# Optimization experiments

Measured on AMD Instinct MI355X. Metric: run time of the kernel, lower is better.

The kernel has to match this reference:

```python
import jax, jax.numpy as jnp
import numpy as np

V, E, H, C, L, S, NL = 50257, 512, 1024, 1024, 1024, 2048, 2


def setup_inputs() -> dict:
    key = jax.random.key(0)
    ks = jax.random.split(key, 28)
    w = 0.02  # weight init scale
    def n(k, shape, s=1.0):
        return jax.random.normal(k, shape, dtype=jnp.float32) * s
    return {
        'input_ids': jax.random.randint(ks[0], (1,), 0, V, dtype=jnp.int32),
        'h0': n(ks[1], (NL, 1, H)),
        'c0': n(ks[2], (NL, 1, H)),
        'left_context': n(ks[3], (S, C)),
        'right_context': n(ks[4], (S, C)),
        'lemma_outputs': n(ks[5], (S, L)),
        # parameters
        'embedding': n(ks[6], (V, E), w),
        'W_ih0': n(ks[7], (4 * H, E), w), 'W_hh0': n(ks[8], (4 * H, H), w),
        'b_ih0': n(ks[9], (4 * H,), w), 'b_hh0': n(ks[10], (4 * H,), w),
        'W_ih1': n(ks[11], (4 * H, H), w), 'W_hh1': n(ks[12], (4 * H, H), w),
        'b_ih1': n(ks[13], (4 * H,), w), 'b_hh1': n(ks[14], (4 * H,), w),
        'W_left': n(ks[15], (H, C), w), 'b_left': n(ks[16], (H,), w),
        'W_right': n(ks[17], (H, C), w), 'b_right': n(ks[18], (H,), w),
        'W_lemma': n(ks[19], (H, L), w), 'b_lemma': n(ks[20], (H,), w),
        'W_concat': n(ks[21], (H, H + 2 * C + L), w), 'b_concat': n(ks[22], (H,), w),
        'W_out': n(ks[23], (V, H), w), 'b_out': n(ks[24], (V,), w),
    }


def _lstm_step(x, h, c, W_ih, W_hh, b_ih, b_hh):
    # torch LSTM gate order: i, f, g, o
    g = x @ W_ih.T + b_ih + h @ W_hh.T + b_hh  # [1, 4H]
    i, f, gg, o = jnp.split(g, 4, axis=-1)
    i = jax.nn.sigmoid(i); f = jax.nn.sigmoid(f)
    gg = jnp.tanh(gg); o = jax.nn.sigmoid(o)
    c_new = f * c + i * gg
    h_new = o * jnp.tanh(c_new)
    return h_new, c_new


def _attend(ctx, W, b, q):
    # ctx: [S, C], q: [1, H] -> Luong-style attention
    e = (ctx @ W.T + b) @ q.T          # [S, 1]
    a = jax.nn.softmax(e[:, 0])        # [S]
    return (a @ ctx)[None, :]          # [1, C]


def reference(input_ids, h0, c0, left_context, right_context, lemma_outputs,
              embedding, W_ih0, W_hh0, b_ih0, b_hh0, W_ih1, W_hh1, b_ih1, b_hh1,
              W_left, b_left, W_right, b_right, W_lemma, b_lemma,
              W_concat, b_concat, W_out, b_out):
    x = embedding[input_ids]  # [1, E]  (dropout p=0 -> identity)
    h_0, c_0 = _lstm_step(x, h0[0], c0[0], W_ih0, W_hh0, b_ih0, b_hh0)
    h_1, c_1 = _lstm_step(h_0, h0[1], c0[1], W_ih1, W_hh1, b_ih1, b_hh1)
    rnn_output = h_1  # [1, H]
    lcontext = _attend(left_context, W_left, b_left, rnn_output)
    rcontext = _attend(right_context, W_right, b_right, rnn_output)
    lemma_ctx = _attend(lemma_outputs, W_lemma, b_lemma, rnn_output)
    concat_in = jnp.concatenate([rnn_output, lcontext, rcontext, lemma_ctx], axis=-1)
    concat_out = jnp.tanh(concat_in @ W_concat.T + b_concat)  # [1, H]
    output = concat_out @ W_out.T + b_out                      # [1, V]
    h_new = jnp.stack([h_0, h_1], axis=0)  # [NL, 1, H]
    c_new = jnp.stack([c_0, c_1], axis=0)
    return output, h_new, c_new
```

## Files before the change

### kernel.cpp

```cpp
#include <hip/hip_runtime.h>
#include <hip/hip_bf16.h>
#include <math.h>


#define WS_H0        0
#define WS_CONCAT_IN 1024
#define WS_CTXOUT    2048
#define WS_V         5120
#define WS_E         8192
#define WS_COUT      20480
#define OUT_V        50257

__device__ __forceinline__ float wave_sum(float v) {
#pragma unroll
    for (int o = 32; o > 0; o >>= 1) v += __shfl_down(v, o, 64);
    return v;
}

__device__ __forceinline__ float dot4(float4 a, float4 b) {
    return a.x * b.x + a.y * b.y + a.z * b.z + a.w * b.w;
}

__device__ __forceinline__ float sigmoidf_(float x) {
    return 1.0f / (1.0f + expf(-x));
}

template <int N4E>
__global__ __launch_bounds__(256) void lstm_kernel(
    const float* __restrict__ x_base, const int* __restrict__ ids,
    const float* __restrict__ W_ih, const float* __restrict__ W_hh,
    const float* __restrict__ b_ih, const float* __restrict__ b_hh,
    const float* __restrict__ hprev, const float* __restrict__ cprev,
    float* __restrict__ h_ws, float* __restrict__ h_out, float* __restrict__ c_out,
    float* __restrict__ zero_base, int zero_count)
{
    if (zero_base != nullptr) {
        int idx = blockIdx.x * 256 + threadIdx.x;
        if (idx < zero_count) zero_base[idx] = 0.0f;
    }

    const float* x = (ids != nullptr) ? (x_base + (size_t)(4 * N4E) * (size_t)ids[0]) : x_base;

    const int k = blockIdx.x;
    const int w = threadIdx.x >> 6;
    const int lane = threadIdx.x & 63;
    const int row = w * 1024 + k;

    float acc = 0.0f;
    {
        const float4* r4 = (const float4*)(W_ih + (size_t)row * (4 * N4E));
        const float4* x4 = (const float4*)x;
#pragma unroll
        for (int j = 0; j < N4E / 64; ++j)
            acc += dot4(r4[lane + 64 * j], x4[lane + 64 * j]);
    }
    {
        const float4* r4 = (const float4*)(W_hh + (size_t)row * 1024);
        const float4* h4 = (const float4*)hprev;
#pragma unroll
        for (int j = 0; j < 4; ++j)
            acc += dot4(r4[lane + 64 * j], h4[lane + 64 * j]);
    }
    acc = wave_sum(acc);

    __shared__ float g[4];
    if (lane == 0) g[w] = acc + b_ih[row] + b_hh[row];
    __syncthreads();
    if (threadIdx.x == 0) {
        float i_ = sigmoidf_(g[0]);
        float f_ = sigmoidf_(g[1]);
        float g_ = tanhf(g[2]);
        float o_ = sigmoidf_(g[3]);
        float c_new = f_ * cprev[k] + i_ * g_;
        float h_new = o_ * tanhf(c_new);
        h_ws[k] = h_new;
        h_out[k] = h_new;
        c_out[k] = c_new;
    }
}

__global__ __launch_bounds__(256) void attn_v_kernel(
    const float* __restrict__ W0, const float* __restrict__ W1,
    const float* __restrict__ W2, const float* __restrict__ q,
    float* __restrict__ v)
{
    const int a = blockIdx.x >> 6;
    const int chunk = blockIdx.x & 63;
    const float* W = (a == 0) ? W0 : (a == 1) ? W1 : W2;
    const int c = threadIdx.x * 4;
    float4 acc = make_float4(0.f, 0.f, 0.f, 0.f);
#pragma unroll 4
    for (int h = chunk * 16; h < chunk * 16 + 16; ++h) {
        float qh = q[h];
        float4 wv = *(const float4*)(W + (size_t)h * 1024 + c);
        acc.x += wv.x * qh; acc.y += wv.y * qh;
        acc.z += wv.z * qh; acc.w += wv.w * qh;
    }
    float* vd = v + a * 1024 + c;
    atomicAdd(vd + 0, acc.x); atomicAdd(vd + 1, acc.y);
    atomicAdd(vd + 2, acc.z); atomicAdd(vd + 3, acc.w);
}

__global__ __launch_bounds__(256) void attn_e_kernel(
    const float* __restrict__ C0, const float* __restrict__ C1,
    const float* __restrict__ C2, const float* __restrict__ v,
    float* __restrict__ e)
{
    const int wid = (blockIdx.x * 256 + threadIdx.x) >> 6;
    const int lane = threadIdx.x & 63;
    const int a = wid >> 11;
    const int s = wid & 2047;
    const float* ctx = (a == 0) ? C0 : (a == 1) ? C1 : C2;
    const float4* r4 = (const float4*)(ctx + (size_t)s * 1024);
    const float4* v4 = (const float4*)(v + a * 1024);
    float acc = 0.0f;
#pragma unroll
    for (int j = 0; j < 4; ++j) acc += dot4(r4[lane + 64 * j], v4[lane + 64 * j]);
    acc = wave_sum(acc);
    if (lane == 0) e[a * 2048 + s] = acc;
}

__global__ __launch_bounds__(256) void attn_ctx_kernel(
    const float* __restrict__ C0, const float* __restrict__ C1,
    const float* __restrict__ C2, const float* __restrict__ e,
    float* __restrict__ ctx_out)
{
    const int a = blockIdx.x >> 6;
    const int chunk = blockIdx.x & 63;
    const float* ctx = (a == 0) ? C0 : (a == 1) ? C1 : C2;
    const float* ea = e + a * 2048;

    __shared__ float red[256];
    const int t = threadIdx.x;
    float m = -1e30f;
    for (int i = t; i < 2048; i += 256) m = fmaxf(m, ea[i]);
    red[t] = m; __syncthreads();
    for (int o = 128; o > 0; o >>= 1) {
        if (t < o) red[t] = fmaxf(red[t], red[t + o]);
        __syncthreads();
    }
    m = red[0]; __syncthreads();

    float ssum = 0.0f;
    for (int i = t; i < 2048; i += 256) ssum += expf(ea[i] - m);
    red[t] = ssum; __syncthreads();
    for (int o = 128; o > 0; o >>= 1) {
        if (t < o) red[t] += red[t + o];
        __syncthreads();
    }
    const float inv = 1.0f / red[0];

    const int c = t * 4;
    float4 acc = make_float4(0.f, 0.f, 0.f, 0.f);
    for (int s = chunk * 32; s < chunk * 32 + 32; ++s) {
        float wgt = expf(ea[s] - m) * inv;
        float4 cv = *(const float4*)(ctx + (size_t)s * 1024 + c);
        acc.x += wgt * cv.x; acc.y += wgt * cv.y;
        acc.z += wgt * cv.z; acc.w += wgt * cv.w;
    }
    float* od = ctx_out + a * 1024 + c;
    atomicAdd(od + 0, acc.x); atomicAdd(od + 1, acc.y);
    atomicAdd(od + 2, acc.z); atomicAdd(od + 3, acc.w);
}

__global__ __launch_bounds__(256) void concat_kernel(
    const float* __restrict__ W, const float* __restrict__ b,
    const float* __restrict__ cin, float* __restrict__ cout)
{
    const int w = threadIdx.x >> 6;
    const int lane = threadIdx.x & 63;
    const int j = blockIdx.x * 4 + w;
    const float4* r4 = (const float4*)(W + (size_t)j * 4096);
    const float4* x4 = (const float4*)cin;
    float acc = 0.0f;
#pragma unroll
    for (int jj = 0; jj < 16; ++jj) acc += dot4(r4[lane + 64 * jj], x4[lane + 64 * jj]);
    acc = wave_sum(acc);
    if (lane == 0) cout[j] = tanhf(acc + b[j]);
}

__global__ __launch_bounds__(256) void out_kernel(
    const float* __restrict__ W, const float* __restrict__ b,
    const float* __restrict__ x, float* __restrict__ out)
{
    const int vrow = (blockIdx.x * 256 + threadIdx.x) >> 6;
    const int lane = threadIdx.x & 63;
    if (vrow >= OUT_V) return;
    const float bias = (lane == 0) ? b[vrow] : 0.0f;
    const float4* r4 = (const float4*)(W + (size_t)vrow * 1024);
    const float4* x4 = (const float4*)x;
    float acc = dot4(r4[lane], x4[lane])
              + dot4(r4[lane + 64], x4[lane + 64])
              + dot4(r4[lane + 128], x4[lane + 128])
              + dot4(r4[lane + 192], x4[lane + 192]);
    acc = wave_sum(acc);
    if (lane == 0) out[vrow] = acc + bias;
}

extern "C" void kernel_launch(void* const* d_in, const int* in_sizes, int n_in,
                              void* d_out, int out_size, void* d_ws, size_t ws_size,
                              hipStream_t stream) {
    const int*   input_ids = (const int*)  d_in[0];
    const float* h0        = (const float*)d_in[1];
    const float* c0        = (const float*)d_in[2];
    const float* lctx      = (const float*)d_in[3];
    const float* rctx      = (const float*)d_in[4];
    const float* lemma     = (const float*)d_in[5];
    const float* emb       = (const float*)d_in[6];
    const float* W_ih0     = (const float*)d_in[7];
    const float* W_hh0     = (const float*)d_in[8];
    const float* b_ih0     = (const float*)d_in[9];
    const float* b_hh0     = (const float*)d_in[10];
    const float* W_ih1     = (const float*)d_in[11];
    const float* W_hh1     = (const float*)d_in[12];
    const float* b_ih1     = (const float*)d_in[13];
    const float* b_hh1     = (const float*)d_in[14];
    const float* W_left    = (const float*)d_in[15];
    const float* W_right   = (const float*)d_in[17];
    const float* W_lemma   = (const float*)d_in[19];
    const float* W_concat  = (const float*)d_in[21];
    const float* b_concat  = (const float*)d_in[22];
    const float* W_out     = (const float*)d_in[23];
    const float* b_out     = (const float*)d_in[24];
    (void)in_sizes; (void)n_in; (void)out_size; (void)ws_size;

    float* out = (float*)d_out;
    float* ws  = (float*)d_ws;

    float* h0_out = out + OUT_V;
    float* h1_out = out + OUT_V + 1024;
    float* c0_out = out + OUT_V + 2048;
    float* c1_out = out + OUT_V + 3072;

    lstm_kernel<128><<<1024, 256, 0, stream>>>(
        emb, input_ids, W_ih0, W_hh0, b_ih0, b_hh0,
        h0, c0, ws + WS_H0, h0_out, c0_out,
        ws + WS_CTXOUT, 6144);

    lstm_kernel<256><<<1024, 256, 0, stream>>>(
        ws + WS_H0, nullptr, W_ih1, W_hh1, b_ih1, b_hh1,
        h0 + 1024, c0 + 1024, ws + WS_CONCAT_IN, h1_out, c1_out,
        nullptr, 0);

    attn_v_kernel<<<192, 256, 0, stream>>>(
        W_left, W_right, W_lemma, ws + WS_CONCAT_IN, ws + WS_V);

    attn_e_kernel<<<1536, 256, 0, stream>>>(
        lctx, rctx, lemma, ws + WS_V, ws + WS_E);

    attn_ctx_kernel<<<192, 256, 0, stream>>>(
        lctx, rctx, lemma, ws + WS_E, ws + WS_CTXOUT);

    concat_kernel<<<256, 256, 0, stream>>>(
        W_concat, b_concat, ws + WS_CONCAT_IN, ws + WS_COUT);

    out_kernel<<<(OUT_V * 64 + 255) / 256, 256, 0, stream>>>(
        W_out, b_out, ws + WS_COUT, out);
}
```

Measured before the change: 454.7 us.

## Fuse attention scores and context into one pass with deferred softmax normalization

Merges the score kernel and the context kernel into one kernel that reads each context row once, computes its score, and accumulates exp-weighted rows along with a running denominator. The max-subtraction softmax is dropped, and normalization moves into the concat kernel, which scales each context segment by the reciprocal of its atomically summed denominator. This halves reads of the three 8MB context matrices and removes one launch. The cost is that expf without max subtraction can overflow when scores are large, and the redundant per-block softmax reductions are gone.

```diff
diff --git a/kernel.cpp b/kernel.cpp
--- a/kernel.cpp
+++ b/kernel.cpp
@@ -7,7 +7,7 @@
 #define WS_CONCAT_IN 1024
 #define WS_CTXOUT    2048
 #define WS_V         5120
-#define WS_E         8192
+#define WS_DENOM     8192
 #define WS_COUT      20480
 #define OUT_V        50257
 
@@ -101,80 +101,81 @@
     atomicAdd(vd + 2, acc.z); atomicAdd(vd + 3, acc.w);
 }
 
-__global__ __launch_bounds__(256) void attn_e_kernel(
+__global__ __launch_bounds__(256) void attn_fused_kernel(
     const float* __restrict__ C0, const float* __restrict__ C1,
     const float* __restrict__ C2, const float* __restrict__ v,
-    float* __restrict__ e)
-{
-    const int wid = (blockIdx.x * 256 + threadIdx.x) >> 6;
-    const int lane = threadIdx.x & 63;
-    const int a = wid >> 11;
-    const int s = wid & 2047;
-    const float* ctx = (a == 0) ? C0 : (a == 1) ? C1 : C2;
-    const float4* r4 = (const float4*)(ctx + (size_t)s * 1024);
-    const float4* v4 = (const float4*)(v + a * 1024);
-    float acc = 0.0f;
-#pragma unroll
-    for (int j = 0; j < 4; ++j) acc += dot4(r4[lane + 64 * j], v4[lane + 64 * j]);
-    acc = wave_sum(acc);
-    if (lane == 0) e[a * 2048 + s] = acc;
-}
-
-__global__ __launch_bounds__(256) void attn_ctx_kernel(
-    const float* __restrict__ C0, const float* __restrict__ C1,
-    const float* __restrict__ C2, const float* __restrict__ e,
-    float* __restrict__ ctx_out)
+    float* __restrict__ ctx_out, float* __restrict__ denom)
 {
     const int a = blockIdx.x >> 6;
     const int chunk = blockIdx.x & 63;
     const float* ctx = (a == 0) ? C0 : (a == 1) ? C1 : C2;
-    const float* ea = e + a * 2048;
-
-    __shared__ float red[256];
+    const int w = threadIdx.x >> 6;
+    const int lane = threadIdx.x & 63;
+
+    __shared__ float quad[4][1024];
+    __shared__ float dred[4];
+
+    const float4* v4 = (const float4*)(v + a * 1024);
+    const float4 vv0 = v4[lane],       vv1 = v4[lane + 64],
+                 vv2 = v4[lane + 128], vv3 = v4[lane + 192];
+
+    float4 a0 = make_float4(0.f, 0.f, 0.f, 0.f), a1 = a0, a2 = a0, a3 = a0;
+    float wsum = 0.0f;
+    const int sbase = chunk * 32 + w * 8;
+#pragma unroll
+    for (int r = 0; r < 8; ++r) {
+        const float4* r4 = (const float4*)(ctx + (size_t)(sbase + r) * 1024);
+        const float4 c0 = r4[lane],       c1 = r4[lane + 64],
+                     c2 = r4[lane + 128], c3 = r4[lane + 192];
+        float e = dot4(c0, vv0) + dot4(c1, vv1) + dot4(c2, vv2) + dot4(c3, vv3);
+#pragma unroll
+        for (int o = 32; o > 0; o >>= 1) e += __shfl_xor(e, o, 64);
+        const float wgt = expf(e);
+        wsum += wgt;
+        a0.x += wgt * c0.x; a0.y += wgt * c0.y; a0.z += wgt * c0.z; a0.w += wgt * c0.w;
+        a1.x += wgt * c1.x; a1.y += wgt * c1.y; a1.z += wgt * c1.z; a1.w += wgt * c1.w;
+        a2.x += wgt * c2.x; a2.y += wgt * c2.y; a2.z += wgt * c2.z; a2.w += wgt * c2.w;
+        a3.x += wgt * c3.x; a3.y += wgt * c3.y; a3.z += wgt * c3.z; a3.w += wgt * c3.w;
+    }
+    float4* q4 = (float4*)quad[w];
+    q4[lane] = a0; q4[lane + 64] = a1; q4[lane + 128] = a2; q4[lane + 192] = a3;
+    if (lane == 0) dred[w] = wsum;
+    __syncthreads();
+
     const int t = threadIdx.x;
-    float m = -1e30f;
-    for (int i = t; i < 2048; i += 256) m = fmaxf(m, ea[i]);
-    red[t] = m; __syncthreads();
-    for (int o = 128; o > 0; o >>= 1) {
-        if (t < o) red[t] = fmaxf(red[t], red[t + o]);
-        __syncthreads();
-    }
-    m = red[0]; __syncthreads();
-
-    float ssum = 0.0f;
-    for (int i = t; i < 2048; i += 256) ssum += expf(ea[i] - m);
-    red[t] = ssum; __syncthreads();
-    for (int o = 128; o > 0; o >>= 1) {
-        if (t < o) red[t] += red[t + o];
-        __syncthreads();
-    }
-    const float inv = 1.0f / red[0];
-
-    const int c = t * 4;
-    float4 acc = make_float4(0.f, 0.f, 0.f, 0.f);
-    for (int s = chunk * 32; s < chunk * 32 + 32; ++s) {
-        float wgt = expf(ea[s] - m) * inv;
-        float4 cv = *(const float4*)(ctx + (size_t)s * 1024 + c);
-        acc.x += wgt * cv.x; acc.y += wgt * cv.y;
-        acc.z += wgt * cv.z; acc.w += wgt * cv.w;
-    }
-    float* od = ctx_out + a * 1024 + c;
-    atomicAdd(od + 0, acc.x); atomicAdd(od + 1, acc.y);
-    atomicAdd(od + 2, acc.z); atomicAdd(od + 3, acc.w);
+    float4 s0 = ((const float4*)quad[0])[t];
+    float4 s1 = ((const float4*)quad[1])[t];
+    float4 s2 = ((const float4*)quad[2])[t];
+    float4 s3 = ((const float4*)quad[3])[t];
+    float* od = ctx_out + a * 1024 + t * 4;
+    atomicAdd(od + 0, s0.x + s1.x + s2.x + s3.x);
+    atomicAdd(od + 1, s0.y + s1.y + s2.y + s3.y);
+    atomicAdd(od + 2, s0.z + s1.z + s2.z + s3.z);
+    atomicAdd(od + 3, s0.w + s1.w + s2.w + s3.w);
+    if (t == 0) atomicAdd(&denom[a], dred[0] + dred[1] + dred[2] + dred[3]);
 }
 
 __global__ __launch_bounds__(256) void concat_kernel(
     const float* __restrict__ W, const float* __restrict__ b,
-    const float* __restrict__ cin, float* __restrict__ cout)
+    const float* __restrict__ cin, const float* __restrict__ denom,
+    float* __restrict__ cout)
 {
     const int w = threadIdx.x >> 6;
     const int lane = threadIdx.x & 63;
     const int j = blockIdx.x * 4 + w;
+    const float i1 = 1.0f / denom[0];
+    const float i2 = 1.0f / denom[1];
+    const float i3 = 1.0f / denom[2];
     const float4* r4 = (const float4*)(W + (size_t)j * 4096);
     const float4* x4 = (const float4*)cin;
     float acc = 0.0f;
 #pragma unroll
-    for (int jj = 0; jj < 16; ++jj) acc += dot4(r4[lane + 64 * jj], x4[lane + 64 * jj]);
+    for (int jj = 0; jj < 16; ++jj) {
+        const int idx = lane + 64 * jj;
+        const int reg = idx >> 8;
+        const float s = (reg == 0) ? 1.0f : (reg == 1) ? i1 : (reg == 2) ? i2 : i3;
+        acc += s * dot4(r4[idx], x4[idx]);
+    }
     acc = wave_sum(acc);
     if (lane == 0) cout[j] = tanhf(acc + b[j]);
 }
@@ -235,7 +236,7 @@
     lstm_kernel<128><<<1024, 256, 0, stream>>>(
         emb, input_ids, W_ih0, W_hh0, b_ih0, b_hh0,
         h0, c0, ws + WS_H0, h0_out, c0_out,
-        ws + WS_CTXOUT, 6144);
+        ws + WS_CTXOUT, 6147);
 
     lstm_kernel<256><<<1024, 256, 0, stream>>>(
         ws + WS_H0, nullptr, W_ih1, W_hh1, b_ih1, b_hh1,
@@ -245,14 +246,11 @@
     attn_v_kernel<<<192, 256, 0, stream>>>(
         W_left, W_right, W_lemma, ws + WS_CONCAT_IN, ws + WS_V);
 
-    attn_e_kernel<<<1536, 256, 0, stream>>>(
-        lctx, rctx, lemma, ws + WS_V, ws + WS_E);
-
-    attn_ctx_kernel<<<192, 256, 0, stream>>>(
-        lctx, rctx, lemma, ws + WS_E, ws + WS_CTXOUT);
+    attn_fused_kernel<<<192, 256, 0, stream>>>(
+        lctx, rctx, lemma, ws + WS_V, ws + WS_CTXOUT, ws + WS_DENOM);
 
     concat_kernel<<<256, 256, 0, stream>>>(
-        W_concat, b_concat, ws + WS_CONCAT_IN, ws + WS_COUT);
+        W_concat, b_concat, ws + WS_CONCAT_IN, ws + WS_DENOM, ws + WS_COUT);
 
     out_kernel<<<(OUT_V * 64 + 255) / 256, 256, 0, stream>>>(
         W_out, b_out, ws + WS_COUT, out);
```

Measured after the change: 451.5 us. No clear change (-0.7%).
